# Kernel optimization log

Hardware: AMD Instinct MI355X
Metric: run time of the kernel (lower is better)

## Reference

```python
import jax, jax.numpy as jnp
import numpy as np

N_NODES = 20000
N_EDGES = 160000
D_IN = 512
D_OUT = 64


def _propagate(x, src, dst, num_nodes):
    # SLPropagate with add_self_loops=False, normalize=False:
    # out[dst] += x[src]  (plain sum aggregation over incoming edges)
    return jax.ops.segment_sum(x[src], dst, num_segments=num_nodes)


def setup_inputs() -> dict:
    key = jax.random.key(0)
    k1, k2, k3, k4 = jax.random.split(key, 4)
    x = jax.random.normal(k1, (N_NODES, D_IN), dtype=jnp.float32)
    edge_index = jax.random.randint(k2, (2, N_EDGES), 0, N_NODES, dtype=jnp.int64)
    # torch.nn.Linear default init scale ~ 1/sqrt(fan_in)
    s = 1.0 / np.sqrt(D_IN)
    W1 = jax.random.uniform(k3, (D_IN, D_IN), dtype=jnp.float32, minval=-s, maxval=s)
    W2 = jax.random.uniform(k4, (D_OUT, D_IN), dtype=jnp.float32, minval=-s, maxval=s)
    return {"x": x, "edge_index": edge_index, "W1": W1, "W2": W2}


def reference(x, edge_index, W1, W2):
    num_nodes = x.shape[0]
    src, dst = edge_index[0], edge_index[1]
    h = _propagate(x, src, dst, num_nodes)          # [N, D_IN]
    h = jax.nn.relu(jnp.einsum('nd,ed->ne', h, W1))  # lin1 (no bias) + relu
    h = _propagate(h, src, dst, num_nodes)          # [N, D_IN]
    h = jnp.einsum('nd,od->no', h, W2)              # lin2 (no bias) -> [N, D_OUT]
    return jax.nn.log_softmax(h, axis=1)
```

## Files before the change

kernel.cpp:

```cpp
#include <hip/hip_runtime.h>

#define D 512
#define DOUT 64
#define MAXDEG 64

typedef __bf16 bf16x8 __attribute__((ext_vector_type(8)));
typedef float floatx4 __attribute__((ext_vector_type(4)));

__device__ __forceinline__ void async_cp16(const void* g, void* lds) {
    __builtin_amdgcn_global_load_lds(
        (__attribute__((address_space(1))) void*)(void*)g,
        (__attribute__((address_space(3))) void*)lds, 16, 0, 0);
}

__global__ __launch_bounds__(256) void prep_kernel(
        int* __restrict__ cnt, int nN, int zeroBlocks,
        __bf16* __restrict__ tzero,
        const float* __restrict__ x, __bf16* __restrict__ xb, int xN8,
        const float* __restrict__ W1, __bf16* __restrict__ w1b, int w1N8,
        const float* __restrict__ W2, __bf16* __restrict__ w2b, int w2N8) {
    int b = blockIdx.x;
    if (b < zeroBlocks) {
        int i4 = b * 1024 + threadIdx.x * 4;
        if (i4 + 3 < nN) *(int4*)(cnt + i4) = make_int4(0, 0, 0, 0);
        else {
            if (i4 + 0 < nN) cnt[i4 + 0] = 0;
            if (i4 + 1 < nN) cnt[i4 + 1] = 0;
            if (i4 + 2 < nN) cnt[i4 + 2] = 0;
        }
        return;
    }
    b -= zeroBlocks;
    if (b == 0) {
        ((unsigned*)tzero)[threadIdx.x] = 0u;
        return;
    }
    b -= 1;
    int xBlocks = (xN8 + 255) >> 8;
    int w1Blocks = (w1N8 + 255) >> 8;
    const float* in; __bf16* outp; int n8;
    if (b < xBlocks) { in = x; outp = xb; n8 = xN8; }
    else if (b < xBlocks + w1Blocks) { b -= xBlocks; in = W1; outp = w1b; n8 = w1N8; }
    else { b -= xBlocks + w1Blocks; in = W2; outp = w2b; n8 = w2N8; }
    int i = b * 256 + threadIdx.x;
    if (i < n8) {
        const float4* p = (const float4*)in + (size_t)i * 2;
        float4 v0 = p[0], v1 = p[1];
        bf16x8 o;
        o[0] = (__bf16)v0.x; o[1] = (__bf16)v0.y; o[2] = (__bf16)v0.z; o[3] = (__bf16)v0.w;
        o[4] = (__bf16)v1.x; o[5] = (__bf16)v1.y; o[6] = (__bf16)v1.z; o[7] = (__bf16)v1.w;
        *((bf16x8*)outp + i) = o;
    }
}

__global__ __launch_bounds__(256) void gemm1_fill(
        const __bf16* __restrict__ A, const __bf16* __restrict__ B,
        __bf16* __restrict__ Cout, int M, int gemmBlocks,
        const int* __restrict__ src, const int* __restrict__ dst,
        int* __restrict__ cnt, int* __restrict__ col, int nE) {
    if (blockIdx.x >= gemmBlocks) {
        int base = (blockIdx.x - gemmBlocks) * 256 + threadIdx.x;
        int stride = (gridDim.x - gemmBlocks) * 256;
        for (int e = base; e < nE; e += stride) {
            int d = dst[e];
            int slot = atomicAdd(&cnt[d], 1);
            if (slot < MAXDEG) col[(size_t)d * MAXDEG + slot] = src[e];
        }
        return;
    }
    constexpr int BM = 128, BN = 128, BK = 64;
    __shared__ __bf16 As[8 * BM * 8];
    __shared__ __bf16 Bs[8 * BN * 8];

    const int tid = threadIdx.x;
    const int w = tid >> 6, lane = tid & 63;
    const int wrow = w >> 1, wcol = w & 1;
    const int m0 = (blockIdx.x >> 2) * BM, n0 = (blockIdx.x & 3) * BN;
    const int quad = lane >> 4, l15 = lane & 15;

    const int srow = lane >> 3;
    const int skq  = (lane & 7) ^ (srow & 7);

    floatx4 acc[4][4] = {};

    for (int k0 = 0; k0 < D; k0 += BK) {
        #pragma unroll
        for (int c = 0; c < 4; ++c) {
            int P0 = (w * 4 + c) * 64;
            int r  = (P0 >> 3) + srow;
            int gr = m0 + r; if (gr > M - 1) gr = M - 1;
            async_cp16(A + (size_t)gr * D + k0 + skq * 8, &As[(size_t)P0 * 8]);
        }
        #pragma unroll
        for (int c = 0; c < 4; ++c) {
            int P0 = (w * 4 + c) * 64;
            int nn = n0 + (P0 >> 3) + srow;
            async_cp16(B + (size_t)nn * D + k0 + skq * 8, &Bs[(size_t)P0 * 8]);
        }
        __syncthreads();

        #pragma unroll
        for (int ksub = 0; ksub < 2; ++ksub) {
            const int kk = ksub * 4 + quad;
            bf16x8 af[4], bfr[4];
            #pragma unroll
            for (int mi = 0; mi < 4; ++mi) {
                int row = wrow * 64 + mi * 16 + l15;
                af[mi] = *(const bf16x8*)&As[(size_t)(row * 8 + (kk ^ (row & 7))) * 8];
            }
            #pragma unroll
            for (int nj = 0; nj < 4; ++nj) {
                int row = wcol * 64 + nj * 16 + l15;
                bfr[nj] = *(const bf16x8*)&Bs[(size_t)(row * 8 + (kk ^ (row & 7))) * 8];
            }
            #pragma unroll
            for (int mi = 0; mi < 4; ++mi)
                #pragma unroll
                for (int nj = 0; nj < 4; ++nj)
                    acc[mi][nj] = __builtin_amdgcn_mfma_f32_16x16x32_bf16(
                        af[mi], bfr[nj], acc[mi][nj], 0, 0, 0);
        }
        __syncthreads();
    }

    #pragma unroll
    for (int mi = 0; mi < 4; ++mi) {
        #pragma unroll
        for (int r = 0; r < 4; ++r) {
            int m = m0 + wrow * 64 + mi * 16 + quad * 4 + r;
            if (m < M) {
                #pragma unroll
                for (int nj = 0; nj < 4; ++nj) {
                    int n = n0 + wcol * 64 + nj * 16 + l15;
                    Cout[(size_t)m * D + n] = (__bf16)acc[mi][nj][r];
                }
            }
        }
    }
}

__global__ __launch_bounds__(256) void prop1_gemm2(
        const __bf16* __restrict__ t, const int* __restrict__ cnt,
        const int* __restrict__ col, const __bf16* __restrict__ B,
        __bf16* __restrict__ u, int nN) {
    __shared__ __bf16 As[16 * 512];

    const int tid = threadIdx.x;
    const int w = tid >> 6, lane = tid & 63;
    const int quad = lane >> 4, l15 = lane & 15;
    const int m0 = blockIdx.x * 8;

    int deg[2];
    const int4* ip[2];
    float acc[2][8] = {};
    int maxb = 0;
    #pragma unroll
    for (int q = 0; q < 2; ++q) {
        int n = m0 + w + q * 4;
        int nc = (n < nN) ? n : 0;
        int d = 0;
        if (n < nN) { d = cnt[n]; if (d > MAXDEG) d = MAXDEG; }
        deg[q] = d;
        ip[q] = (const int4*)(col + (size_t)nc * MAXDEG);
        int bq = (d + 3) >> 2;
        if (bq > maxb) maxb = bq;
    }

    for (int b = 0; b < maxb; ++b) {
        int s[2][4];
        #pragma unroll
        for (int q = 0; q < 2; ++q) {
            int4 i4 = ip[q][b];
            int e0 = b * 4;
            s[q][0] = (e0 + 0 < deg[q]) ? i4.x : nN;
            s[q][1] = (e0 + 1 < deg[q]) ? i4.y : nN;
            s[q][2] = (e0 + 2 < deg[q]) ? i4.z : nN;
            s[q][3] = (e0 + 3 < deg[q]) ? i4.w : nN;
        }
        bf16x8 v[2][4];
        #pragma unroll
        for (int q = 0; q < 2; ++q)
            #pragma unroll
            for (int j = 0; j < 4; ++j)
                v[q][j] = *(const bf16x8*)(t + (size_t)s[q][j] * D + lane * 8);
        #pragma unroll
        for (int q = 0; q < 2; ++q)
            #pragma unroll
            for (int i = 0; i < 8; ++i)
                acc[q][i] += ((float)v[q][0][i] + (float)v[q][1][i])
                           + ((float)v[q][2][i] + (float)v[q][3][i]);
    }

    bf16x8 breg[16];
    #pragma unroll
    for (int kq = 0; kq < 16; ++kq)
        breg[kq] = *(const bf16x8*)(B + (size_t)(w * 16 + l15) * D + kq * 32 + quad * 8);

    #pragma unroll
    for (int q = 0; q < 2; ++q) {
        int r = w + q * 4;
        bf16x8 o;
        #pragma unroll
        for (int i = 0; i < 8; ++i) o[i] = (__bf16)fmaxf(acc[q][i], 0.f);
        int P = r * 64 + ((lane + r) & 63);
        *(bf16x8*)&As[(size_t)P * 8] = o;
    }
    __syncthreads();

    floatx4 c = {};
    #pragma unroll
    for (int kq = 0; kq < 16; ++kq) {
        int g = kq * 4 + quad;
        bf16x8 af = *(const bf16x8*)&As[(size_t)(l15 * 64 + ((g + l15) & 63)) * 8];
        c = __builtin_amdgcn_mfma_f32_16x16x32_bf16(af, breg[kq], c, 0, 0, 0);
    }

    #pragma unroll
    for (int r = 0; r < 4; ++r) {
        int row = quad * 4 + r;
        int m = m0 + row;
        if (row < 8 && m < nN)
            u[(size_t)m * DOUT + w * 16 + l15] = (__bf16)c[r];
    }
}

__global__ __launch_bounds__(256) void prop2_lsm(const __bf16* __restrict__ u,
        const int* __restrict__ cnt, const int* __restrict__ col,
        float* __restrict__ out, int nN) {
    int n = blockIdx.x * 4 + (threadIdx.x >> 6);
    if (n >= nN) return;
    int lane = threadIdx.x & 63;
    int deg = cnt[n]; if (deg > MAXDEG) deg = MAXDEG;
    const int* cp = col + (size_t)n * MAXDEG;
    float a0 = 0.f, a1 = 0.f, a2 = 0.f, a3 = 0.f;
    float a4 = 0.f, a5 = 0.f, a6 = 0.f, a7 = 0.f;
    int e = 0;
    for (; e + 8 <= deg; e += 8) {
        int s0 = cp[e],     s1 = cp[e + 1], s2 = cp[e + 2], s3 = cp[e + 3];
        int s4 = cp[e + 4], s5 = cp[e + 5], s6 = cp[e + 6], s7 = cp[e + 7];
        a0 += (float)u[(size_t)s0 * DOUT + lane];
        a1 += (float)u[(size_t)s1 * DOUT + lane];
        a2 += (float)u[(size_t)s2 * DOUT + lane];
        a3 += (float)u[(size_t)s3 * DOUT + lane];
        a4 += (float)u[(size_t)s4 * DOUT + lane];
        a5 += (float)u[(size_t)s5 * DOUT + lane];
        a6 += (float)u[(size_t)s6 * DOUT + lane];
        a7 += (float)u[(size_t)s7 * DOUT + lane];
    }
    for (; e + 4 <= deg; e += 4) {
        int s0 = cp[e], s1 = cp[e + 1], s2 = cp[e + 2], s3 = cp[e + 3];
        a0 += (float)u[(size_t)s0 * DOUT + lane];
        a1 += (float)u[(size_t)s1 * DOUT + lane];
        a2 += (float)u[(size_t)s2 * DOUT + lane];
        a3 += (float)u[(size_t)s3 * DOUT + lane];
    }
    for (; e < deg; ++e) a0 += (float)u[(size_t)cp[e] * DOUT + lane];
    float v = ((a0 + a4) + (a1 + a5)) + ((a2 + a6) + (a3 + a7));
    float mx = v;
    #pragma unroll
    for (int off = 32; off >= 1; off >>= 1) mx = fmaxf(mx, __shfl_xor(mx, off, 64));
    float s = expf(v - mx);
    #pragma unroll
    for (int off = 32; off >= 1; off >>= 1) s += __shfl_xor(s, off, 64);
    out[(size_t)n * DOUT + lane] = v - mx - logf(s);
}


extern "C" void kernel_launch(void* const* d_in, const int* in_sizes, int n_in,
                              void* d_out, int out_size, void* d_ws, size_t ws_size,
                              hipStream_t stream) {
    const float* x  = (const float*)d_in[0];
    const int*   ei = (const int*)d_in[1];
    const float* W1 = (const float*)d_in[2];
    const float* W2 = (const float*)d_in[3];
    float* out = (float*)d_out;

    const int N = in_sizes[0] / D;
    const int E = in_sizes[1] / 2;
    const int* src = ei;
    const int* dst = ei + E;

    size_t off = 0;
    auto alloc = [&](size_t bytes) -> void* {
        void* p = (char*)d_ws + off;
        off = (off + bytes + 255) & ~(size_t)255;
        return p;
    };
    int*    cnt     = (int*)alloc(sizeof(int) * (size_t)N);
    int*    col     = (int*)alloc(sizeof(int) * (size_t)N * MAXDEG);
    __bf16* w1b     = (__bf16*)alloc(sizeof(__bf16) * (size_t)D * D);
    __bf16* w2b     = (__bf16*)alloc(sizeof(__bf16) * (size_t)DOUT * D);
    __bf16* xb      = (__bf16*)alloc(sizeof(__bf16) * (size_t)N * D);
    __bf16* t       = (__bf16*)alloc(sizeof(__bf16) * (size_t)(N + 1) * D);
    __bf16* u       = (__bf16*)alloc(sizeof(__bf16) * (size_t)N * DOUT);

    const int zeroBlocks = (N + 1023) / 1024;
    const int xN8 = N * D / 8, w1N8 = D * D / 8, w2N8 = DOUT * D / 8;
    const int cvtBlocks = (xN8 + 255) / 256 + (w1N8 + 255) / 256 + (w2N8 + 255) / 256;

    prep_kernel<<<zeroBlocks + 1 + cvtBlocks, 256, 0, stream>>>(
        cnt, N, zeroBlocks, t + (size_t)N * D, x, xb, xN8, W1, w1b, w1N8, W2, w2b, w2N8);

    const int gemmBlocks = ((N + 127) / 128) * 4;
    gemm1_fill<<<gemmBlocks + 64, 256, 0, stream>>>(
        xb, w1b, t, N, gemmBlocks, src, dst, cnt, col, E);

    prop1_gemm2<<<(N + 7) / 8, 256, 0, stream>>>(t, cnt, col, w2b, u, N);

    prop2_lsm<<<(N + 3) / 4, 256, 0, stream>>>(u, cnt, col, out, N);
}
```

Baseline: 161.3 us.

## Fuse fp32-to-bf16 conversion of x into gemm1 A-tile loads with XCD remap

Removes the separate pass that converted x to bf16 (one read of fp32 x plus a write and re-read of bf16 xb). gemm1 now streams fp32 x directly into LDS with a 16-way XOR swizzle and converts to bf16 in registers before the MFMA. It also remaps block indices so neighbouring tiles land on the same XCD, and adds a min-blocks hint to launch_bounds. This doubles the LDS footprint for A and the global bytes gemm1 reads for A, and adds conversion work to the inner loop.

Result: faster. 155.4 us (-3.6%).

```diff
diff --git a/kernel.cpp b/kernel.cpp
--- a/kernel.cpp
+++ b/kernel.cpp
@@ -16,7 +16,6 @@
 __global__ __launch_bounds__(256) void prep_kernel(
         int* __restrict__ cnt, int nN, int zeroBlocks,
         __bf16* __restrict__ tzero,
-        const float* __restrict__ x, __bf16* __restrict__ xb, int xN8,
         const float* __restrict__ W1, __bf16* __restrict__ w1b, int w1N8,
         const float* __restrict__ W2, __bf16* __restrict__ w2b, int w2N8) {
     int b = blockIdx.x;
@@ -36,12 +35,10 @@
         return;
     }
     b -= 1;
-    int xBlocks = (xN8 + 255) >> 8;
     int w1Blocks = (w1N8 + 255) >> 8;
     const float* in; __bf16* outp; int n8;
-    if (b < xBlocks) { in = x; outp = xb; n8 = xN8; }
-    else if (b < xBlocks + w1Blocks) { b -= xBlocks; in = W1; outp = w1b; n8 = w1N8; }
-    else { b -= xBlocks + w1Blocks; in = W2; outp = w2b; n8 = w2N8; }
+    if (b < w1Blocks) { in = W1; outp = w1b; n8 = w1N8; }
+    else { b -= w1Blocks; in = W2; outp = w2b; n8 = w2N8; }
     int i = b * 256 + threadIdx.x;
     if (i < n8) {
         const float4* p = (const float4*)in + (size_t)i * 2;
@@ -53,8 +50,8 @@
     }
 }
 
-__global__ __launch_bounds__(256) void gemm1_fill(
-        const __bf16* __restrict__ A, const __bf16* __restrict__ B,
+__global__ __launch_bounds__(256, 3) void gemm1_fill(
+        const float* __restrict__ Af, const __bf16* __restrict__ B,
         __bf16* __restrict__ Cout, int M, int gemmBlocks,
         const int* __restrict__ src, const int* __restrict__ dst,
         int* __restrict__ cnt, int* __restrict__ col, int nE) {
@@ -68,14 +65,18 @@
         }
         return;
     }
-    constexpr int BM = 128, BN = 128, BK = 64;
-    __shared__ __bf16 As[8 * BM * 8];
+    constexpr int BM = 128, BN = 128;
+    __shared__ float  Asf[BM * 16 * 4];
     __shared__ __bf16 Bs[8 * BN * 8];
+
+    const int qch = gemmBlocks >> 3, rch = gemmBlocks & 7;
+    const int xcd = blockIdx.x & 7, jj = blockIdx.x >> 3;
+    const int L = (xcd < rch ? xcd * (qch + 1) : rch * (qch + 1) + (xcd - rch) * qch) + jj;
 
     const int tid = threadIdx.x;
     const int w = tid >> 6, lane = tid & 63;
     const int wrow = w >> 1, wcol = w & 1;
-    const int m0 = (blockIdx.x >> 2) * BM, n0 = (blockIdx.x & 3) * BN;
+    const int m0 = (L >> 2) * BM, n0 = (L & 3) * BN;
     const int quad = lane >> 4, l15 = lane & 15;
 
     const int srow = lane >> 3;
@@ -83,13 +84,15 @@
 
     floatx4 acc[4][4] = {};
 
-    for (int k0 = 0; k0 < D; k0 += BK) {
-        #pragma unroll
-        for (int c = 0; c < 4; ++c) {
-            int P0 = (w * 4 + c) * 64;
-            int r  = (P0 >> 3) + srow;
-            int gr = m0 + r; if (gr > M - 1) gr = M - 1;
-            async_cp16(A + (size_t)gr * D + k0 + skq * 8, &As[(size_t)P0 * 8]);
+    for (int k0 = 0; k0 < D; k0 += 64) {
+        #pragma unroll
+        for (int c = 0; c < 8; ++c) {
+            int P0 = (w * 8 + c) * 64;
+            int P = P0 + lane;
+            int rloc = P >> 4, cu = P & 15;
+            int gr = m0 + rloc; if (gr > M - 1) gr = M - 1;
+            async_cp16(Af + (size_t)gr * D + k0 + ((cu ^ (rloc & 15)) << 2),
+                       &Asf[(size_t)P0 * 4]);
         }
         #pragma unroll
         for (int c = 0; c < 4; ++c) {
@@ -105,8 +108,17 @@
             bf16x8 af[4], bfr[4];
             #pragma unroll
             for (int mi = 0; mi < 4; ++mi) {
-                int row = wrow * 64 + mi * 16 + l15;
-                af[mi] = *(const bf16x8*)&As[(size_t)(row * 8 + (kk ^ (row & 7))) * 8];
+                int rr = wrow * 64 + mi * 16 + l15;
+                int u0 = ((kk << 1)    ) ^ (rr & 15);
+                int u1 = ((kk << 1) | 1) ^ (rr & 15);
+                float4 f0 = *(const float4*)&Asf[(size_t)(rr * 16 + u0) * 4];
+                float4 f1 = *(const float4*)&Asf[(size_t)(rr * 16 + u1) * 4];
+                bf16x8 a_;
+                a_[0] = (__bf16)f0.x; a_[1] = (__bf16)f0.y;
+                a_[2] = (__bf16)f0.z; a_[3] = (__bf16)f0.w;
+                a_[4] = (__bf16)f1.x; a_[5] = (__bf16)f1.y;
+                a_[6] = (__bf16)f1.z; a_[7] = (__bf16)f1.w;
+                af[mi] = a_;
             }
             #pragma unroll
             for (int nj = 0; nj < 4; ++nj) {
@@ -290,20 +302,19 @@
     int*    col     = (int*)alloc(sizeof(int) * (size_t)N * MAXDEG);
     __bf16* w1b     = (__bf16*)alloc(sizeof(__bf16) * (size_t)D * D);
     __bf16* w2b     = (__bf16*)alloc(sizeof(__bf16) * (size_t)DOUT * D);
-    __bf16* xb      = (__bf16*)alloc(sizeof(__bf16) * (size_t)N * D);
     __bf16* t       = (__bf16*)alloc(sizeof(__bf16) * (size_t)(N + 1) * D);
     __bf16* u       = (__bf16*)alloc(sizeof(__bf16) * (size_t)N * DOUT);
 
     const int zeroBlocks = (N + 1023) / 1024;
-    const int xN8 = N * D / 8, w1N8 = D * D / 8, w2N8 = DOUT * D / 8;
-    const int cvtBlocks = (xN8 + 255) / 256 + (w1N8 + 255) / 256 + (w2N8 + 255) / 256;
+    const int w1N8 = D * D / 8, w2N8 = DOUT * D / 8;
+    const int cvtBlocks = (w1N8 + 255) / 256 + (w2N8 + 255) / 256;
 
     prep_kernel<<<zeroBlocks + 1 + cvtBlocks, 256, 0, stream>>>(
-        cnt, N, zeroBlocks, t + (size_t)N * D, x, xb, xN8, W1, w1b, w1N8, W2, w2b, w2N8);
+        cnt, N, zeroBlocks, t + (size_t)N * D, W1, w1b, w1N8, W2, w2b, w2N8);
 
     const int gemmBlocks = ((N + 127) / 128) * 4;
     gemm1_fill<<<gemmBlocks + 64, 256, 0, stream>>>(
-        xb, w1b, t, N, gemmBlocks, src, dst, cnt, col, E);
+        x, w1b, t, N, gemmBlocks, src, dst, cnt, col, E);
 
     prop1_gemm2<<<(N + 7) / 8, 256, 0, stream>>>(t, cnt, col, w2b, u, N);
 
```
